# Performance work log

Measured on AMD Instinct MI355X. Metric: run time of the kernel, lower is better.

The kernel has to match this reference:

```python
import jax, jax.numpy as jnp
import numpy as np
from jax import lax

EPS = 1e-6
K1D = 3  # DACA conv1d kernel size for C=64


def binquant(x):
    # forward of BinaryQuantize_Quad (sign); STE only matters for bwd
    return jnp.sign(x)


def daca(x, w1d):
    # x: [B,C,H,W] -> per-channel sigmoid gate [B,C,1,1]
    b, c, h, w = x.shape
    flat = x.reshape(b, c, h * w)
    ch_mean = flat.mean(axis=2)
    ch_var = flat.var(axis=2, ddof=1) + EPS  # torch.var default unbiased=True
    ch_std = jnp.sqrt(ch_var)
    ch_abs = jnp.abs(flat).mean(axis=2)  # adaptive avg pool of |x|
    y = jnp.stack([ch_abs, ch_mean, ch_std], axis=1)  # [B,3,C]
    y = lax.conv_general_dilated(
        y, w1d, window_strides=(1,), padding=[(K1D // 2, K1D // 2)],
        dimension_numbers=("NCH", "OIH", "NCH"))  # [B,1,C]
    return jax.nn.sigmoid(y[:, 0, :, None, None])  # [B,C,1,1]


def hard_binary_conv(x, w):
    # scaling: mean |w| over (in,kh,kw), per out-channel, detached
    scale = jnp.mean(jnp.abs(w), axis=(1, 2, 3), keepdims=True)
    cw = jnp.clip(w, -1.0, 1.0)
    bw = lax.stop_gradient(scale * jnp.sign(w) - cw) + cw  # value=scale*sign(w), grad via clip
    return lax.conv_general_dilated(
        x, bw, window_strides=(1, 1), padding=[(1, 1), (1, 1)],
        dimension_numbers=("NCHW", "OIHW", "NCHW"))


def rprelu(x, b0, a, b1):
    y = x + b0
    y = jnp.where(y > 0, y, a[None, :, None, None] * y)  # PReLU per-channel
    return y + b1


def setup_inputs() -> dict:
    key = jax.random.key(0)
    ks = jax.random.split(key, 7)
    C = 64
    x = jax.random.normal(ks[0], (8, C, 256, 256), dtype=jnp.float32)
    w_conv = jax.random.normal(ks[1], (C, C, 3, 3), dtype=jnp.float32) * 0.1
    w1d = jax.random.normal(ks[2], (1, 3, K1D), dtype=jnp.float32) * 0.3
    b_move = jax.random.normal(ks[3], (1, C, 1, 1), dtype=jnp.float32) * 0.02
    pr_b0 = jax.random.normal(ks[4], (1, C, 1, 1), dtype=jnp.float32) * 0.02
    prelu_a = jnp.full((C,), 0.25, dtype=jnp.float32)
    pr_b1 = jax.random.normal(ks[5], (1, C, 1, 1), dtype=jnp.float32) * 0.02
    return {"x": x, "b_move": b_move, "w_conv": w_conv, "w1d": w1d,
            "pr_b0": pr_b0, "prelu_a": prelu_a, "pr_b1": pr_b1}


def reference(x, b_move, w_conv, w1d, pr_b0, prelu_a, pr_b1):
    out = x + b_move                 # LearnableBias move0
    scale = daca(out, w1d)           # [B,C,1,1] gate
    out = binquant(out)              # sign binarization of activations
    out = hard_binary_conv(out, w_conv)
    out = out * scale
    out = rprelu(out, pr_b0, prelu_a, pr_b1)
    return out + x                   # residual
```

## Files before the change

kernel.cpp:

```cpp
#include <hip/hip_runtime.h>
#include <stdint.h>

#define BB 8
#define C  64
#define H  256
#define W  256
#define HW (H*W)
#define EPSV 1e-6f

typedef unsigned long long u64;
typedef float __attribute__((ext_vector_type(4))) f32x4;

__global__ __launch_bounds__(256) void k_stats(const float* __restrict__ x,
                                               const float* __restrict__ bmove,
                                               float* __restrict__ sums ) {
  int bc = blockIdx.x;
  float bm = bmove[bc & 63];
  const f32x4* p = (const f32x4*)(x + (size_t)bc * HW);
  int t = threadIdx.x;
  float s = 0.f, s2 = 0.f, sa = 0.f;
  #pragma unroll 8
  for (int k = 0; k < 64; ++k) {
    f32x4 v = p[(k << 8) | t];
    float a0 = v.x + bm, a1 = v.y + bm, a2 = v.z + bm, a3 = v.w + bm;
    s  += a0 + a1 + a2 + a3;
    s2 += a0*a0 + a1*a1 + a2*a2 + a3*a3;
    sa += fabsf(a0) + fabsf(a1) + fabsf(a2) + fabsf(a3);
  }
  #pragma unroll
  for (int off = 32; off > 0; off >>= 1) {
    s  += __shfl_down(s,  off, 64);
    s2 += __shfl_down(s2, off, 64);
    sa += __shfl_down(sa, off, 64);
  }
  __shared__ float red[4][3];
  int wid = t >> 6;
  if ((t & 63) == 0) { red[wid][0] = s; red[wid][1] = s2; red[wid][2] = sa; }
  __syncthreads();
  if (t == 0) {
    float S  = red[0][0] + red[1][0] + red[2][0] + red[3][0];
    float S2 = red[0][1] + red[1][1] + red[2][1] + red[3][1];
    float SA = red[0][2] + red[1][2] + red[2][2] + red[3][2];
    sums[bc] = S; sums[512 + bc] = S2; sums[1024 + bc] = SA;
  }
}

__global__ __launch_bounds__(256) void k_pack(const float* __restrict__ x,
                                              const float* __restrict__ bmove,
                                              u64* __restrict__ packed) {
  int blk = blockIdx.x;
  int b   = blk >> 7;
  int rg  = blk & 127;
  int h0  = rg << 1;
  int tid = threadIdx.x;
  int wid = tid >> 6, lane = tid & 63;
  __shared__ f32x4 lds4[64 * 33];

  float bm = bmove[lane];
  int p4l = tid & 31;
  int cg  = tid >> 5;
  const size_t bbase = (size_t)b * C * HW;

  for (int tile = 0; tile < 4; ++tile) {
    int h  = h0 + (tile >> 1);
    int wb = (tile & 1) << 7;
    __syncthreads();
    #pragma unroll
    for (int cc = 0; cc < 8; ++cc) {
      int c = cg + (cc << 3);
      lds4[c * 33 + p4l] =
          *((const f32x4*)(x + bbase + (size_t)c * HW + h * W + wb) + p4l);
    }
    __syncthreads();
    u64* pdst = packed + ((size_t)(b * H + h)) * W + wb;
    #pragma unroll
    for (int k = 0; k < 8; ++k) {
      int p4i = (wid << 3) + k;
      f32x4 v = lds4[lane * 33 + p4i];
      u64 q0 = __ballot(v.x + bm > 0.f);
      u64 q1 = __ballot(v.y + bm > 0.f);
      u64 q2 = __ballot(v.z + bm > 0.f);
      u64 q3 = __ballot(v.w + bm > 0.f);
      u64 qa = (lane & 1) ? q1 : q0;
      u64 qb = (lane & 1) ? q3 : q2;
      u64 qq = (lane & 2) ? qb : qa;
      if (lane < 4) pdst[(p4i << 2) + lane] = qq;
    }
  }
}

__global__ __launch_bounds__(512) void k_gate(const float* __restrict__ sums,
                                              const float* __restrict__ w_conv,
                                              const float* __restrict__ w1d,
                                              float* __restrict__ alpha,
                                              u64* __restrict__ wsign) {
  __shared__ float stA[512], stM[512], stS[512];
  __shared__ float swv[64];
  int tid = threadIdx.x;
  {
    float s = sums[tid], s2 = sums[512 + tid], sa = sums[1024 + tid];
    const float invN = 1.f / (float)HW;
    float mean = s * invN;
    float var  = (s2 - s * s * invN) * (1.f / (float)(HW - 1)) + EPSV;
    stA[tid] = sa * invN;
    stM[tid] = mean;
    stS[tid] = sqrtf(var);
  }
  {
    int o = tid >> 3, g = tid & 7;
    const float* wo = w_conv + o * 576 + g * 72;
    float s = 0.f;
    u64 wb[9] = {0,0,0,0,0,0,0,0,0};
    #pragma unroll
    for (int i = 0; i < 8; i++) {
      #pragma unroll
      for (int tp = 0; tp < 9; tp++) {
        float v = wo[i * 9 + tp];
        s += fabsf(v);
        if (v > 0.f) wb[tp] |= (1ull << (g * 8 + i));
      }
    }
    #pragma unroll
    for (int off = 4; off > 0; off >>= 1) {
      s += __shfl_down(s, off, 8);
      #pragma unroll
      for (int tp = 0; tp < 9; tp++)
        wb[tp] |= __shfl_down(wb[tp], off, 8);
    }
    if (g == 0) {
      swv[o] = s * (1.f / 576.f);
      #pragma unroll
      for (int tp = 0; tp < 9; tp++) wsign[o * 9 + tp] = wb[tp];
    }
  }
  __syncthreads();
  int b = tid >> 6, c = tid & 63;
  float y = 0.f;
  #pragma unroll
  for (int k = 0; k < 3; k++) {
    int cc = c + k - 1;
    if (cc >= 0 && cc < 64) {
      int j = b * 64 + cc;
      y += stA[j] * w1d[0 * 3 + k] + stM[j] * w1d[1 * 3 + k] + stS[j] * w1d[2 * 3 + k];
    }
  }
  float gate = 1.f / (1.f + expf(-y));
  alpha[tid] = gate * swv[c];
}

__global__ __launch_bounds__(256) void k_conv4(const u64* __restrict__ packed,
                                               const u64* __restrict__ wsign,
                                               const float* __restrict__ alpha,
                                               const float* __restrict__ x,
                                               const float* __restrict__ pr_b0,
                                               const float* __restrict__ prelu_a,
                                               const float* __restrict__ pr_b1,
                                               float* __restrict__ out) {
  int blk = blockIdx.x;
  int oq = blk & 3;
  int hg = (blk >> 2) & 63;
  int b  = blk >> 8;
  int h0 = hg << 2;
  int t = threadIdx.x;
  __shared__ u64 rows[6][W];
  const u64* pb = packed + (size_t)b * H * W;
  #pragma unroll
  for (int r = 0; r < 6; ++r) {
    int hr = h0 - 1 + r;
    rows[r][t] = (hr >= 0 && hr < H) ? pb[hr * W + t] : 0ull;
  }
  __syncthreads();

  int tr = t >> 6, lane = t & 63;
  int tw = lane << 2;
  int h  = h0 + tr;
  bool rTop = (h > 0), rBot = (h < H - 1);
  u64 vm0 = (lane == 0)  ? 0ull : ~0ull;
  u64 vm5 = (lane == 63) ? 0ull : ~0ull;

  u64 nw[3][6];
  #pragma unroll
  for (int rr = 0; rr < 3; ++rr) {
    #pragma unroll
    for (int j = 0; j < 6; ++j) {
      int wi = tw - 1 + j;
      wi = (wi < 0) ? 0 : (wi > W - 1 ? W - 1 : wi);
      nw[rr][j] = rows[tr + rr][wi];
    }
  }
  int nr = 1 + (int)rTop + (int)rBot;
  float base0 = 64.f * (float)nr * ((lane == 0)  ? 2.f : 3.f);
  float base1 = 64.f * (float)nr * 3.f;
  float base3 = 64.f * (float)nr * ((lane == 63) ? 2.f : 3.f);

  int o0 = oq << 4;
  size_t xoff = (size_t)b * C * HW + (size_t)(o0) * HW + (size_t)h * W + tw;
  const float* al = alpha + b * 64 + o0;
  const float* pb0 = pr_b0 + o0;
  const float* ppa = prelu_a + o0;
  const float* pb1 = pr_b1 + o0;
  const u64* wsq = wsign + (size_t)o0 * 9;

  #pragma unroll 2
  for (int oo = 0; oo < 16; ++oo) {
    const u64* ws = wsq + oo * 9;
    u64 w0=ws[0], w1=ws[1], w2=ws[2], w3=ws[3], w4=ws[4],
        w5=ws[5], w6=ws[6], w7=ws[7], w8=ws[8];
    f32x4 xr = *(const f32x4*)(x + xoff + (size_t)oo * HW);
    int c0 = 0, c1 = 0, c2 = 0, c3 = 0;
    if (rTop) {
      c0 += __popcll((nw[0][0]^w0)&vm0) + __popcll(nw[0][1]^w1) + __popcll(nw[0][2]^w2);
      c1 += __popcll(nw[0][1]^w0) + __popcll(nw[0][2]^w1) + __popcll(nw[0][3]^w2);
      c2 += __popcll(nw[0][2]^w0) + __popcll(nw[0][3]^w1) + __popcll(nw[0][4]^w2);
      c3 += __popcll(nw[0][3]^w0) + __popcll(nw[0][4]^w1) + __popcll((nw[0][5]^w2)&vm5);
    }
    {
      c0 += __popcll((nw[1][0]^w3)&vm0) + __popcll(nw[1][1]^w4) + __popcll(nw[1][2]^w5);
      c1 += __popcll(nw[1][1]^w3) + __popcll(nw[1][2]^w4) + __popcll(nw[1][3]^w5);
      c2 += __popcll(nw[1][2]^w3) + __popcll(nw[1][3]^w4) + __popcll(nw[1][4]^w5);
      c3 += __popcll(nw[1][3]^w3) + __popcll(nw[1][4]^w4) + __popcll((nw[1][5]^w5)&vm5);
    }
    if (rBot) {
      c0 += __popcll((nw[2][0]^w6)&vm0) + __popcll(nw[2][1]^w7) + __popcll(nw[2][2]^w8);
      c1 += __popcll(nw[2][1]^w6) + __popcll(nw[2][2]^w7) + __popcll(nw[2][3]^w8);
      c2 += __popcll(nw[2][2]^w6) + __popcll(nw[2][3]^w7) + __popcll(nw[2][4]^w8);
      c3 += __popcll(nw[2][3]^w6) + __popcll(nw[2][4]^w7) + __popcll((nw[2][5]^w8)&vm5);
    }
    float a  = al[oo];
    float b0 = pb0[oo], pa = ppa[oo], b1 = pb1[oo];
    float d0 = (base0 - 2.f*(float)c0) * a + b0;
    float d1 = (base1 - 2.f*(float)c1) * a + b0;
    float d2 = (base1 - 2.f*(float)c2) * a + b0;
    float d3 = (base3 - 2.f*(float)c3) * a + b0;
    d0 = (d0 > 0.f) ? d0 : pa * d0;
    d1 = (d1 > 0.f) ? d1 : pa * d1;
    d2 = (d2 > 0.f) ? d2 : pa * d2;
    d3 = (d3 > 0.f) ? d3 : pa * d3;
    f32x4 ov;
    ov.x = d0 + b1 + xr.x;
    ov.y = d1 + b1 + xr.y;
    ov.z = d2 + b1 + xr.z;
    ov.w = d3 + b1 + xr.w;
    __builtin_nontemporal_store(ov, (f32x4*)(out + xoff + (size_t)oo * HW));
  }
}

extern "C" void kernel_launch(void* const* d_in, const int* in_sizes, int n_in,
                              void* d_out, int out_size, void* d_ws, size_t ws_size,
                              hipStream_t stream) {
  const float* x       = (const float*)d_in[0];
  const float* b_move  = (const float*)d_in[1];
  const float* w_conv  = (const float*)d_in[2];
  const float* w1d     = (const float*)d_in[3];
  const float* pr_b0   = (const float*)d_in[4];
  const float* prelu_a = (const float*)d_in[5];
  const float* pr_b1   = (const float*)d_in[6];
  float* out = (float*)d_out;

  char* ws = (char*)d_ws;
  u64*   packed = (u64*)ws;
  float* sums   = (float*)(ws + 4194304);
  float* alpha  = (float*)(ws + 4194304 + 8192);
  u64*   wsign  = (u64*)(ws + 4194304 + 16384);

  k_stats<<<512, 256, 0, stream>>>(x, b_move, sums);
  k_pack<<<1024, 256, 0, stream>>>(x, b_move, packed);
  k_gate<<<1, 512, 0, stream>>>(sums, w_conv, w1d, alpha, wsign);
  k_conv4<<<2048, 256, 0, stream>>>(packed, wsign, alpha, x,
                                    pr_b0, prelu_a, pr_b1, out);
}
```

Baseline: 106.2 us.

## Replace LDS-staged bit packing with ballot plus in-register 64x64 bit transpose

The sign-packing kernel no longer stages tiles of x through shared memory with barriers. Each wavefront now loads four consecutive pixels per lane for each of the 64 channels and ballots the signs, so lane c holds channel c's bits across the wavefront's 256 pixels. A six-stage butterfly shuffle transposes these 64x64 bit matrices so each lane ends up with the per-pixel channel masks, which it writes with 128-bit stores. This removes LDS traffic and synchronisation, at the cost of more cross-lane shuffles, a serial 64-step channel loop per wave, and half as many blocks.

```diff
diff --git a/kernel.cpp b/kernel.cpp
--- a/kernel.cpp
+++ b/kernel.cpp
@@ -10,6 +10,7 @@
 
 typedef unsigned long long u64;
 typedef float __attribute__((ext_vector_type(4))) f32x4;
+typedef unsigned long long __attribute__((ext_vector_type(2))) u64x2;
 
 __global__ __launch_bounds__(256) void k_stats(const float* __restrict__ x,
                                                const float* __restrict__ bmove,
@@ -45,48 +46,48 @@
   }
 }
 
-__global__ __launch_bounds__(256) void k_pack(const float* __restrict__ x,
-                                              const float* __restrict__ bmove,
-                                              u64* __restrict__ packed) {
-  int blk = blockIdx.x;
-  int b   = blk >> 7;
-  int rg  = blk & 127;
-  int h0  = rg << 1;
-  int tid = threadIdx.x;
-  int wid = tid >> 6, lane = tid & 63;
-  __shared__ f32x4 lds4[64 * 33];
-
-  float bm = bmove[lane];
-  int p4l = tid & 31;
-  int cg  = tid >> 5;
-  const size_t bbase = (size_t)b * C * HW;
-
-  for (int tile = 0; tile < 4; ++tile) {
-    int h  = h0 + (tile >> 1);
-    int wb = (tile & 1) << 7;
-    __syncthreads();
-    #pragma unroll
-    for (int cc = 0; cc < 8; ++cc) {
-      int c = cg + (cc << 3);
-      lds4[c * 33 + p4l] =
-          *((const f32x4*)(x + bbase + (size_t)c * HW + h * W + wb) + p4l);
-    }
-    __syncthreads();
-    u64* pdst = packed + ((size_t)(b * H + h)) * W + wb;
-    #pragma unroll
-    for (int k = 0; k < 8; ++k) {
-      int p4i = (wid << 3) + k;
-      f32x4 v = lds4[lane * 33 + p4i];
-      u64 q0 = __ballot(v.x + bm > 0.f);
-      u64 q1 = __ballot(v.y + bm > 0.f);
-      u64 q2 = __ballot(v.z + bm > 0.f);
-      u64 q3 = __ballot(v.w + bm > 0.f);
-      u64 qa = (lane & 1) ? q1 : q0;
-      u64 qb = (lane & 1) ? q3 : q2;
-      u64 qq = (lane & 2) ? qb : qa;
-      if (lane < 4) pdst[(p4i << 2) + lane] = qq;
-    }
-  }
+__global__ __launch_bounds__(256) void k_packT(const float* __restrict__ x,
+                                               const float* __restrict__ bmove,
+                                               u64* __restrict__ packed) {
+  int gw   = (blockIdx.x << 2) + (threadIdx.x >> 6);
+  int lane = threadIdx.x & 63;
+  int b    = gw >> 8;
+  int px0  = (gw & 255) << 8;
+  const float* xb = x + (size_t)b * C * HW + px0 + (lane << 2);
+
+  u64 r0 = 0, r1 = 0, r2 = 0, r3 = 0;
+  #pragma unroll 8
+  for (int c = 0; c < 64; ++c) {
+    f32x4 v = *(const f32x4*)(xb + (size_t)c * HW);
+    float bm = bmove[c];
+    u64 b0 = __ballot(v.x + bm > 0.f);
+    u64 b1 = __ballot(v.y + bm > 0.f);
+    u64 b2 = __ballot(v.z + bm > 0.f);
+    u64 b3 = __ballot(v.w + bm > 0.f);
+    if (lane == c) { r0 = b0; r1 = b1; r2 = b2; r3 = b3; }
+  }
+  const u64 M[6] = {0x5555555555555555ull, 0x3333333333333333ull,
+                    0x0F0F0F0F0F0F0F0Full, 0x00FF00FF00FF00FFull,
+                    0x0000FFFF0000FFFFull, 0x00000000FFFFFFFFull};
+  #pragma unroll
+  for (int st = 0; st < 6; ++st) {
+    int d = 1 << st;
+    u64 m = M[st];
+    u64 t0 = __shfl_xor(r0, d, 64);
+    u64 t1 = __shfl_xor(r1, d, 64);
+    u64 t2 = __shfl_xor(r2, d, 64);
+    u64 t3 = __shfl_xor(r3, d, 64);
+    bool hi = (lane & d) != 0;
+    r0 = hi ? ((r0 & ~m) | ((t0 & ~m) >> d)) : ((r0 & m) | ((t0 & m) << d));
+    r1 = hi ? ((r1 & ~m) | ((t1 & ~m) >> d)) : ((r1 & m) | ((t1 & m) << d));
+    r2 = hi ? ((r2 & ~m) | ((t2 & ~m) >> d)) : ((r2 & m) | ((t2 & m) << d));
+    r3 = hi ? ((r3 & ~m) | ((t3 & ~m) >> d)) : ((r3 & m) | ((t3 & m) << d));
+  }
+  u64* dst = packed + ((size_t)b << 16) + px0 + (lane << 2);
+  u64x2 s01; s01.x = r0; s01.y = r1;
+  u64x2 s23; s23.x = r2; s23.y = r3;
+  *(u64x2*)dst = s01;
+  *(u64x2*)(dst + 2) = s23;
 }
 
 __global__ __launch_bounds__(512) void k_gate(const float* __restrict__ sums,
@@ -264,7 +265,7 @@
   u64*   wsign  = (u64*)(ws + 4194304 + 16384);
 
   k_stats<<<512, 256, 0, stream>>>(x, b_move, sums);
-  k_pack<<<1024, 256, 0, stream>>>(x, b_move, packed);
+  k_packT<<<512, 256, 0, stream>>>(x, b_move, packed);
   k_gate<<<1, 512, 0, stream>>>(sums, w_conv, w1d, alpha, wsign);
   k_conv4<<<2048, 256, 0, stream>>>(packed, wsign, alpha, x,
                                     pr_b0, prelu_a, pr_b1, out);
```

Measured after the change: 112.4 us. 5.8% more time.

## Fuse channel statistics into sign-packing kernel with per-row-group partial sums

Applied to the files above, without the earlier changes.

Removes the separate stats kernel and computes sum, sum of squares and abs-sum inside the packing kernel, which already reads x, so x is read from HBM once instead of twice. Partial sums per 2-row group are written to a workspace and reduced in the single-block gate kernel, which now reads 384 floats per (b,c) serially. The LDS tile padding is replaced by an XOR swizzle. This adds serial reduction work in the one-block gate kernel.

```diff
diff --git a/kernel.cpp b/kernel.cpp
--- a/kernel.cpp
+++ b/kernel.cpp
@@ -11,52 +11,24 @@
 typedef unsigned long long u64;
 typedef float __attribute__((ext_vector_type(4))) f32x4;
 
-__global__ __launch_bounds__(256) void k_stats(const float* __restrict__ x,
-                                               const float* __restrict__ bmove,
-                                               float* __restrict__ sums ) {
-  int bc = blockIdx.x;
-  float bm = bmove[bc & 63];
-  const f32x4* p = (const f32x4*)(x + (size_t)bc * HW);
-  int t = threadIdx.x;
-  float s = 0.f, s2 = 0.f, sa = 0.f;
-  #pragma unroll 8
-  for (int k = 0; k < 64; ++k) {
-    f32x4 v = p[(k << 8) | t];
-    float a0 = v.x + bm, a1 = v.y + bm, a2 = v.z + bm, a3 = v.w + bm;
-    s  += a0 + a1 + a2 + a3;
-    s2 += a0*a0 + a1*a1 + a2*a2 + a3*a3;
-    sa += fabsf(a0) + fabsf(a1) + fabsf(a2) + fabsf(a3);
-  }
-  #pragma unroll
-  for (int off = 32; off > 0; off >>= 1) {
-    s  += __shfl_down(s,  off, 64);
-    s2 += __shfl_down(s2, off, 64);
-    sa += __shfl_down(sa, off, 64);
-  }
-  __shared__ float red[4][3];
-  int wid = t >> 6;
-  if ((t & 63) == 0) { red[wid][0] = s; red[wid][1] = s2; red[wid][2] = sa; }
-  __syncthreads();
-  if (t == 0) {
-    float S  = red[0][0] + red[1][0] + red[2][0] + red[3][0];
-    float S2 = red[0][1] + red[1][1] + red[2][1] + red[3][1];
-    float SA = red[0][2] + red[1][2] + red[2][2] + red[3][2];
-    sums[bc] = S; sums[512 + bc] = S2; sums[1024 + bc] = SA;
-  }
-}
-
-__global__ __launch_bounds__(256) void k_pack(const float* __restrict__ x,
-                                              const float* __restrict__ bmove,
-                                              u64* __restrict__ packed) {
+__global__ __launch_bounds__(256) void k_packstats(
+    const float* __restrict__ x,
+    const float* __restrict__ bmove,
+    u64* __restrict__ packed,
+    float* __restrict__ part ) {
   int blk = blockIdx.x;
   int b   = blk >> 7;
   int rg  = blk & 127;
   int h0  = rg << 1;
   int tid = threadIdx.x;
   int wid = tid >> 6, lane = tid & 63;
-  __shared__ f32x4 lds4[64 * 33];
+
+  __shared__ f32x4 lds4[64 * 32];
+  __shared__ float sred[4][3][64];
 
   float bm = bmove[lane];
+  float s = 0.f, s2 = 0.f, sa = 0.f;
+
   int p4l = tid & 31;
   int cg  = tid >> 5;
   const size_t bbase = (size_t)b * C * HW;
@@ -68,7 +40,7 @@
     #pragma unroll
     for (int cc = 0; cc < 8; ++cc) {
       int c = cg + (cc << 3);
-      lds4[c * 33 + p4l] =
+      lds4[(c << 5) + (p4l ^ (c & 7))] =
           *((const f32x4*)(x + bbase + (size_t)c * HW + h * W + wb) + p4l);
     }
     __syncthreads();
@@ -76,29 +48,47 @@
     #pragma unroll
     for (int k = 0; k < 8; ++k) {
       int p4i = (wid << 3) + k;
-      f32x4 v = lds4[lane * 33 + p4i];
-      u64 q0 = __ballot(v.x + bm > 0.f);
-      u64 q1 = __ballot(v.y + bm > 0.f);
-      u64 q2 = __ballot(v.z + bm > 0.f);
-      u64 q3 = __ballot(v.w + bm > 0.f);
+      f32x4 v = lds4[(lane << 5) + (p4i ^ (lane & 7))];
+      float a0 = v.x + bm, a1 = v.y + bm, a2 = v.z + bm, a3 = v.w + bm;
+      s  += (a0 + a1) + (a2 + a3);
+      s2 += a0*a0 + a1*a1 + a2*a2 + a3*a3;
+      sa += (fabsf(a0) + fabsf(a1)) + (fabsf(a2) + fabsf(a3));
+      u64 q0 = __ballot(a0 > 0.f);
+      u64 q1 = __ballot(a1 > 0.f);
+      u64 q2 = __ballot(a2 > 0.f);
+      u64 q3 = __ballot(a3 > 0.f);
       u64 qa = (lane & 1) ? q1 : q0;
       u64 qb = (lane & 1) ? q3 : q2;
       u64 qq = (lane & 2) ? qb : qa;
       if (lane < 4) pdst[(p4i << 2) + lane] = qq;
     }
   }
-}
-
-__global__ __launch_bounds__(512) void k_gate(const float* __restrict__ sums,
-                                              const float* __restrict__ w_conv,
-                                              const float* __restrict__ w1d,
-                                              float* __restrict__ alpha,
-                                              u64* __restrict__ wsign) {
+  sred[wid][0][lane] = s;
+  sred[wid][1][lane] = s2;
+  sred[wid][2][lane] = sa;
+  __syncthreads();
+  if (tid < 192) {
+    int st = tid >> 6, c = tid & 63;
+    float v = sred[0][st][c] + sred[1][st][c] + sred[2][st][c] + sred[3][st][c];
+    part[((size_t)(b * 64 + c) * 3 + st) * 128 + rg] = v;
+  }
+}
+
+__global__ __launch_bounds__(512) void k_gate(
+    const float* __restrict__ part,
+    const float* __restrict__ w_conv,
+    const float* __restrict__ w1d,
+    float* __restrict__ alpha,
+    u64* __restrict__ wsign) {
   __shared__ float stA[512], stM[512], stS[512];
   __shared__ float swv[64];
   int tid = threadIdx.x;
   {
-    float s = sums[tid], s2 = sums[512 + tid], sa = sums[1024 + tid];
+    const f32x4* p = (const f32x4*)(part + (size_t)tid * 384);
+    float s = 0.f, s2 = 0.f, sa = 0.f;
+    for (int k = 0;  k < 32; k++) { f32x4 v = p[k]; s  += (v.x + v.y) + (v.z + v.w); }
+    for (int k = 32; k < 64; k++) { f32x4 v = p[k]; s2 += (v.x + v.y) + (v.z + v.w); }
+    for (int k = 64; k < 96; k++) { f32x4 v = p[k]; sa += (v.x + v.y) + (v.z + v.w); }
     const float invN = 1.f / (float)HW;
     float mean = s * invN;
     float var  = (s2 - s * s * invN) * (1.f / (float)(HW - 1)) + EPSV;
@@ -259,13 +249,12 @@
 
   char* ws = (char*)d_ws;
   u64*   packed = (u64*)ws;
-  float* sums   = (float*)(ws + 4194304);
-  float* alpha  = (float*)(ws + 4194304 + 8192);
-  u64*   wsign  = (u64*)(ws + 4194304 + 16384);
-
-  k_stats<<<512, 256, 0, stream>>>(x, b_move, sums);
-  k_pack<<<1024, 256, 0, stream>>>(x, b_move, packed);
-  k_gate<<<1, 512, 0, stream>>>(sums, w_conv, w1d, alpha, wsign);
+  float* part   = (float*)(ws + 4194304);
+  float* alpha  = (float*)(ws + 4194304 + 786432);
+  u64*   wsign  = (u64*)(ws + 4194304 + 786432 + 4096);
+
+  k_packstats<<<1024, 256, 0, stream>>>(x, b_move, packed, part);
+  k_gate<<<1, 512, 0, stream>>>(part, w_conv, w1d, alpha, wsign);
   k_conv4<<<2048, 256, 0, stream>>>(packed, wsign, alpha, x,
                                     pr_b0, prelu_a, pr_b1, out);
 }
```

Result: slower. 117.5 us (+10.6%).
